# Kernel tuning notes

Hardware: AMD Instinct MI355X
Metric: run time of the kernel (lower is better)

The kernel has to match this reference:

```python
import jax, jax.numpy as jnp
import numpy as np

D_H = 1024

def _binary_operator(e_i, e_j):
    a_i, kv_i = e_i
    a_j, kv_j = e_j
    return (a_j * a_i, a_j * kv_i + kv_j)

def setup_inputs() -> dict:
    key = jax.random.key(0)
    k1, k2 = jax.random.split(key)
    B, S, D = 4, 4096, 1024
    x = jax.random.normal(k1, (B, S, D), dtype=jnp.float32)
    # nn.Dense default lecun_normal-ish scale; plain scaled normal is fine for a reference
    W = jax.random.normal(k2, (D, 3 * D_H), dtype=jnp.float32) * (1.0 / np.sqrt(D))
    b = jnp.zeros((3 * D_H,), dtype=jnp.float32)
    return {"x": x, "W": W, "b": b}

def reference(x, W, b):
    # projection: (B,S,D) @ (D, 3*d_h)
    proj = jnp.einsum('bsd,dh->bsh', x, W) + b
    inp = jnp.tanh(proj[:, :, :D_H])                 # (B,S,d_h)
    gates = jax.nn.sigmoid(proj[:, :, D_H:])         # (B,S,2*d_h)
    input_gate, output_gate = jnp.split(gates, 2, axis=-1)
    forget_gate = 1.0 - input_gate                   # tied gates
    _, hidden = jax.lax.associative_scan(
        _binary_operator, (forget_gate, inp * input_gate), axis=1)
    return jnp.tanh(hidden) * output_gate            # (B,S,d_h)
```

## Files before the change

### kernel.cpp

```cpp
#include <hip/hip_runtime.h>
#include <hip/hip_bf16.h>
#include <cmath>

typedef _Float16 half8 __attribute__((ext_vector_type(8)));
typedef _Float16 half4 __attribute__((ext_vector_type(4)));
typedef float f32x4 __attribute__((ext_vector_type(4)));

#define M_DIM 16384
#define K_DIM 1024
#define N_DIM 3072
#define S_LEN 4096
#define NCHUNK 64
#define CLEN 64

__device__ __forceinline__ float sigmoid_f(float x) {
    return 1.0f / (1.0f + __expf(-x));
}

__global__ void k_cast_x(const float* __restrict__ x, _Float16* __restrict__ xb) {
    int i = blockIdx.x * blockDim.x + threadIdx.x;
    float4 v = reinterpret_cast<const float4*>(x)[i];
    half4 h;
    h.x = (_Float16)v.x; h.y = (_Float16)v.y;
    h.z = (_Float16)v.z; h.w = (_Float16)v.w;
    reinterpret_cast<half4*>(xb)[i] = h;
}

__global__ void k_cast_w(const float* __restrict__ W, _Float16* __restrict__ Wt) {
    int t = blockIdx.x * blockDim.x + threadIdx.x;
    int n = t >> 10;
    int k = t & 1023;
    Wt[t] = (_Float16)W[(size_t)k * N_DIM + n];
}

__global__ __launch_bounds__(256, 2) void k_gemm(
    const _Float16* __restrict__ A,
    const _Float16* __restrict__ Bt,
    const float* __restrict__ bias,
    _Float16* __restrict__ G)
{
    __shared__ _Float16 As[128 * 64];
    __shared__ _Float16 Bs[128 * 64];

    const int lane = threadIdx.x & 63;
    const int w    = threadIdx.x >> 6;
    const int wr   = w >> 1;
    const int wc   = w & 1;

    const int bid   = blockIdx.x;
    const int tileM = (bid / 24) * 128;
    const int tileN = (bid % 24) * 128;

    f32x4 acc[4][4] = {};

    const int rsub = lane >> 3;
    const int ksub = (lane & 7) * 8;

    for (int kt = 0; kt < 16; ++kt) {
        __syncthreads();
        #pragma unroll
        for (int c = 0; c < 4; ++c) {
            const int row = w * 32 + c * 8 + rsub;
            const _Float16* gA = A  + (size_t)(tileM + row) * K_DIM + kt * 64 + ksub;
            const _Float16* gB = Bt + (size_t)(tileN + row) * K_DIM + kt * 64 + ksub;
            __builtin_amdgcn_global_load_lds(
                (const __attribute__((address_space(1))) void*)gA,
                (__attribute__((address_space(3))) void*)(As + (w * 32 + c * 8) * 64),
                16, 0, 0);
            __builtin_amdgcn_global_load_lds(
                (const __attribute__((address_space(1))) void*)gB,
                (__attribute__((address_space(3))) void*)(Bs + (w * 32 + c * 8) * 64),
                16, 0, 0);
        }
        __syncthreads();

        #pragma unroll
        for (int ks = 0; ks < 2; ++ks) {
            half8 af[4], bf[4];
            #pragma unroll
            for (int i = 0; i < 4; ++i)
                af[i] = *reinterpret_cast<const half8*>(
                    &As[(wr * 64 + i * 16 + (lane & 15)) * 64 + ks * 32 + (lane >> 4) * 8]);
            #pragma unroll
            for (int j = 0; j < 4; ++j)
                bf[j] = *reinterpret_cast<const half8*>(
                    &Bs[(wc * 64 + j * 16 + (lane & 15)) * 64 + ks * 32 + (lane >> 4) * 8]);
            #pragma unroll
            for (int i = 0; i < 4; ++i)
                #pragma unroll
                for (int j = 0; j < 4; ++j)
                    acc[i][j] = __builtin_amdgcn_mfma_f32_16x16x32_f16(
                        af[i], bf[j], acc[i][j], 0, 0, 0);
        }
    }

    #pragma unroll
    for (int j = 0; j < 4; ++j) {
        const int n = tileN + wc * 64 + j * 16 + (lane & 15);
        const float bn = bias[n];
        const bool is_tanh = (n < 1024);
        #pragma unroll
        for (int i = 0; i < 4; ++i) {
            const int mbase = tileM + wr * 64 + i * 16 + (lane >> 4) * 4;
            #pragma unroll
            for (int r = 0; r < 4; ++r) {
                float v = acc[i][j][r] + bn;
                float o = is_tanh ? tanhf(v) : sigmoid_f(v);
                G[(size_t)(mbase + r) * N_DIM + n] = (_Float16)o;
            }
        }
    }
}

__global__ void k_scan1(const _Float16* __restrict__ G,
                        float* __restrict__ sumA, float* __restrict__ sumH) {
    const int gid   = blockIdx.x;
    const int dblk  = gid & 3;
    const int chunk = (gid >> 2) & 63;
    const int b     = gid >> 8;
    const int d     = dblk * 256 + threadIdx.x;

    const _Float16* base = G + (size_t)(b * S_LEN + chunk * CLEN) * N_DIM;
    float A = 1.0f, H = 0.0f;
    #pragma unroll 4
    for (int s = 0; s < CLEN; ++s) {
        float g0 = (float)base[(size_t)s * N_DIM + d];
        float g1 = (float)base[(size_t)s * N_DIM + 1024 + d];
        float a  = 1.0f - g1;
        float kv = g0 * g1;
        H = fmaf(a, H, kv);
        A *= a;
    }
    const int cidx = (b * NCHUNK + chunk) * 1024 + d;
    sumA[cidx] = A;
    sumH[cidx] = H;
}

__global__ void k_scan2(const float* __restrict__ sumA, const float* __restrict__ sumH,
                        float* __restrict__ pref) {
    const int c = blockIdx.x * blockDim.x + threadIdx.x;
    const int b = c >> 10;
    const int d = c & 1023;
    float h = 0.0f;
    #pragma unroll 8
    for (int chunk = 0; chunk < NCHUNK; ++chunk) {
        const int idx = (b * NCHUNK + chunk) * 1024 + d;
        pref[idx] = h;
        h = fmaf(sumA[idx], h, sumH[idx]);
    }
}

__global__ void k_scan3(const _Float16* __restrict__ G,
                        const float* __restrict__ pref,
                        float* __restrict__ out) {
    const int gid   = blockIdx.x;
    const int dblk  = gid & 3;
    const int chunk = (gid >> 2) & 63;
    const int b     = gid >> 8;
    const int d     = dblk * 256 + threadIdx.x;

    const _Float16* base = G + (size_t)(b * S_LEN + chunk * CLEN) * N_DIM;
    float h = pref[(b * NCHUNK + chunk) * 1024 + d];
    #pragma unroll 4
    for (int s = 0; s < CLEN; ++s) {
        float g0 = (float)base[(size_t)s * N_DIM + d];
        float g1 = (float)base[(size_t)s * N_DIM + 1024 + d];
        float g2 = (float)base[(size_t)s * N_DIM + 2048 + d];
        float a  = 1.0f - g1;
        float kv = g0 * g1;
        h = fmaf(a, h, kv);
        out[(size_t)(b * S_LEN + chunk * CLEN + s) * 1024 + d] = tanhf(h) * g2;
    }
}

extern "C" void kernel_launch(void* const* d_in, const int* in_sizes, int n_in,
                              void* d_out, int out_size, void* d_ws, size_t ws_size,
                              hipStream_t stream) {
    const float* x = (const float*)d_in[0];
    const float* W = (const float*)d_in[1];
    const float* b = (const float*)d_in[2];
    float* out = (float*)d_out;

    char* ws = (char*)d_ws;
    _Float16* xb = (_Float16*)ws;
    _Float16* Wt = (_Float16*)(ws + 33554432);
    _Float16* G  = (_Float16*)(ws + 33554432 + 6291456);
    float* sumA  = (float*)(ws + 140509184);
    float* sumH  = sumA + 4096 * NCHUNK;
    float* pref  = sumH + 4096 * NCHUNK;

    k_cast_x<<<16384, 256, 0, stream>>>(x, xb);
    k_cast_w<<<12288, 256, 0, stream>>>(W, Wt);
    k_gemm <<<3072, 256, 0, stream>>>(xb, Wt, b, G);
    k_scan1<<<1024, 256, 0, stream>>>(G, sumA, sumH);
    k_scan2<<<16,   256, 0, stream>>>(sumA, sumH, pref);
    k_scan3<<<1024, 256, 0, stream>>>(G, pref, out);
    (void)in_sizes; (void)n_in; (void)out_size; (void)ws_size;
}
```

Measured before the change: 234.3 us.

## Triple-buffer GEMM with XOR-swizzled LDS, larger tiles, and tiled W transpose

The GEMM moves to 256x128 tiles with 512 threads, a three-slot LDS ring filled by global_load_lds, prefetch two k-steps ahead, and one barrier per step. LDS columns are XOR-swizzled to avoid bank conflicts, block IDs are remapped for L2 locality, and MFMA runs under raised wave priority. The W cast/transpose now goes through a shared-memory tile so both global reads and writes are coalesced. The cost is 144KB of dynamic LDS per block, which limits occupancy, plus more complex vmcnt bookkeeping.

Result: no change. 230.6 us (-1.6%).

```diff
diff --git a/kernel.cpp b/kernel.cpp
--- a/kernel.cpp
+++ b/kernel.cpp
@@ -12,6 +12,13 @@
 #define S_LEN 4096
 #define NCHUNK 64
 #define CLEN 64
+
+#define BM 256
+#define BN 128
+#define BK 64
+#define NT 16
+#define A_E 16384
+#define SLOT_E 24576
 
 __device__ __forceinline__ float sigmoid_f(float x) {
     return 1.0f / (1.0f + __expf(-x));
@@ -27,86 +34,127 @@
 }
 
 __global__ void k_cast_w(const float* __restrict__ W, _Float16* __restrict__ Wt) {
-    int t = blockIdx.x * blockDim.x + threadIdx.x;
-    int n = t >> 10;
-    int k = t & 1023;
-    Wt[t] = (_Float16)W[(size_t)k * N_DIM + n];
-}
-
-__global__ __launch_bounds__(256, 2) void k_gemm(
+    __shared__ float t[64][65];
+    const int k0 = (blockIdx.x / 48) * 64;
+    const int n0 = (blockIdx.x % 48) * 64;
+    const int c  = threadIdx.x & 63;
+    const int r0 = threadIdx.x >> 6;
+    #pragma unroll
+    for (int i = 0; i < 16; ++i) {
+        int r = r0 + i * 4;
+        t[r][c] = W[(size_t)(k0 + r) * N_DIM + n0 + c];
+    }
+    __syncthreads();
+    #pragma unroll
+    for (int i = 0; i < 16; ++i) {
+        int r = r0 + i * 4;
+        Wt[(size_t)(n0 + r) * K_DIM + k0 + c] = (_Float16)t[c][r];
+    }
+}
+
+__global__ __launch_bounds__(512, 2) void k_gemm(
     const _Float16* __restrict__ A,
     const _Float16* __restrict__ Bt,
     const float* __restrict__ bias,
     _Float16* __restrict__ G)
 {
-    __shared__ _Float16 As[128 * 64];
-    __shared__ _Float16 Bs[128 * 64];
-
-    const int lane = threadIdx.x & 63;
-    const int w    = threadIdx.x >> 6;
-    const int wr   = w >> 1;
-    const int wc   = w & 1;
+    extern __shared__ _Float16 lds[];
+
+    const int tid  = threadIdx.x;
+    const int lane = tid & 63;
+    const int wid  = tid >> 6;
+    const int wr   = wid >> 1;
+    const int wc   = wid & 1;
 
     const int bid   = blockIdx.x;
-    const int tileM = (bid / 24) * 128;
-    const int tileN = (bid % 24) * 128;
+    const int wg    = (bid & 7) * 192 + (bid >> 3);
+    const int tileM = (wg / 24) * BM;
+    const int tileN = (wg % 24) * BN;
+
+    const int l3   = lane >> 3;
+    const int c8   = lane & 7;
+    const int scol = ((c8 ^ l3) << 3);
+    const _Float16* gA = A  + (size_t)(tileM + wid * 8 + l3) * K_DIM + scol;
+    const _Float16* gB = Bt + (size_t)(tileN + wid * 8 + l3) * K_DIM + scol;
+
+    const int l15 = lane & 15;
+    const int hi  = lane >> 4;
+    const int swz = (l15 & 7) << 3;
+    const int o0  = (hi * 8)      ^ swz;
+    const int o1  = (32 + hi * 8) ^ swz;
 
     f32x4 acc[4][4] = {};
 
-    const int rsub = lane >> 3;
-    const int ksub = (lane & 7) * 8;
-
-    for (int kt = 0; kt < 16; ++kt) {
-        __syncthreads();
+#define GL(SRC, DST) __builtin_amdgcn_global_load_lds( \
+        (const __attribute__((address_space(1))) void*)(SRC), \
+        (__attribute__((address_space(3))) void*)(DST), 16, 0, 0)
+
+#define STAGE(kt, slot) do { \
+        _Float16* as_ = lds + (slot) * SLOT_E + wid * 512; \
+        _Float16* bs_ = lds + (slot) * SLOT_E + A_E + wid * 512; \
+        const _Float16* ga_ = gA + (size_t)(kt) * BK; \
+        const _Float16* gb_ = gB + (size_t)(kt) * BK; \
+        GL(ga_,                        as_);          \
+        GL(ga_ +  64 * K_DIM,          as_ + 4096);   \
+        GL(ga_ + 128 * K_DIM,          as_ + 8192);   \
+        GL(ga_ + 192 * K_DIM,          as_ + 12288);  \
+        GL(gb_,                        bs_);          \
+        GL(gb_ +  64 * K_DIM,          bs_ + 4096);   \
+    } while (0)
+
+    STAGE(0, 0);
+    STAGE(1, 1);
+    asm volatile("s_waitcnt vmcnt(6)" ::: "memory");
+    __builtin_amdgcn_s_barrier();
+
+    int sC = 0, sS = 2;
+    #pragma unroll 1
+    for (int t = 0; t < NT; ++t) {
+        if (t + 2 < NT) STAGE(t + 2, sS);
+
+        const _Float16* as = lds + sC * SLOT_E + (wr * 64 + l15) * 64;
+        const _Float16* bs = lds + sC * SLOT_E + A_E + (wc * 64 + l15) * 64;
+        half8 a0[4], a1[4], b0[4], b1[4];
         #pragma unroll
-        for (int c = 0; c < 4; ++c) {
-            const int row = w * 32 + c * 8 + rsub;
-            const _Float16* gA = A  + (size_t)(tileM + row) * K_DIM + kt * 64 + ksub;
-            const _Float16* gB = Bt + (size_t)(tileN + row) * K_DIM + kt * 64 + ksub;
-            __builtin_amdgcn_global_load_lds(
-                (const __attribute__((address_space(1))) void*)gA,
-                (__attribute__((address_space(3))) void*)(As + (w * 32 + c * 8) * 64),
-                16, 0, 0);
-            __builtin_amdgcn_global_load_lds(
-                (const __attribute__((address_space(1))) void*)gB,
-                (__attribute__((address_space(3))) void*)(Bs + (w * 32 + c * 8) * 64),
-                16, 0, 0);
+        for (int i = 0; i < 4; ++i) {
+            a0[i] = *(const half8*)(as + i * 1024 + o0);
+            a1[i] = *(const half8*)(as + i * 1024 + o1);
+            b0[i] = *(const half8*)(bs + i * 1024 + o0);
+            b1[i] = *(const half8*)(bs + i * 1024 + o1);
         }
-        __syncthreads();
-
+
+        __builtin_amdgcn_s_setprio(1);
         #pragma unroll
-        for (int ks = 0; ks < 2; ++ks) {
-            half8 af[4], bf[4];
+        for (int i = 0; i < 4; ++i)
             #pragma unroll
-            for (int i = 0; i < 4; ++i)
-                af[i] = *reinterpret_cast<const half8*>(
-                    &As[(wr * 64 + i * 16 + (lane & 15)) * 64 + ks * 32 + (lane >> 4) * 8]);
-            #pragma unroll
-            for (int j = 0; j < 4; ++j)
-                bf[j] = *reinterpret_cast<const half8*>(
-                    &Bs[(wc * 64 + j * 16 + (lane & 15)) * 64 + ks * 32 + (lane >> 4) * 8]);
-            #pragma unroll
-            for (int i = 0; i < 4; ++i)
-                #pragma unroll
-                for (int j = 0; j < 4; ++j)
-                    acc[i][j] = __builtin_amdgcn_mfma_f32_16x16x32_f16(
-                        af[i], bf[j], acc[i][j], 0, 0, 0);
-        }
-    }
+            for (int j = 0; j < 4; ++j) {
+                acc[i][j] = __builtin_amdgcn_mfma_f32_16x16x32_f16(a0[i], b0[j], acc[i][j], 0, 0, 0);
+                acc[i][j] = __builtin_amdgcn_mfma_f32_16x16x32_f16(a1[i], b1[j], acc[i][j], 0, 0, 0);
+            }
+        __builtin_amdgcn_s_setprio(0);
+
+        if (t < NT - 2)       asm volatile("s_waitcnt vmcnt(6)" ::: "memory");
+        else if (t == NT - 2) asm volatile("s_waitcnt vmcnt(0)" ::: "memory");
+        if (t < NT - 1) __builtin_amdgcn_s_barrier();
+
+        if (++sC == 3) sC = 0;
+        if (++sS == 3) sS = 0;
+    }
+#undef STAGE
+#undef GL
 
     #pragma unroll
     for (int j = 0; j < 4; ++j) {
-        const int n = tileN + wc * 64 + j * 16 + (lane & 15);
+        const int n = tileN + wc * 64 + j * 16 + l15;
         const float bn = bias[n];
         const bool is_tanh = (n < 1024);
         #pragma unroll
         for (int i = 0; i < 4; ++i) {
-            const int mbase = tileM + wr * 64 + i * 16 + (lane >> 4) * 4;
+            const int mb = tileM + wr * 64 + i * 16 + hi * 4;
             #pragma unroll
             for (int r = 0; r < 4; ++r) {
                 float v = acc[i][j][r] + bn;
-                float o = is_tanh ? tanhf(v) : sigmoid_f(v);
-                G[(size_t)(mbase + r) * N_DIM + n] = (_Float16)o;
+                G[(size_t)(mb + r) * N_DIM + n] = (_Float16)(is_tanh ? tanhf(v) : sigmoid_f(v));
             }
         }
     }
@@ -190,8 +238,8 @@
     float* pref  = sumH + 4096 * NCHUNK;
 
     k_cast_x<<<16384, 256, 0, stream>>>(x, xb);
-    k_cast_w<<<12288, 256, 0, stream>>>(W, Wt);
-    k_gemm <<<3072, 256, 0, stream>>>(xb, Wt, b, G);
+    k_cast_w<<<768,   256, 0, stream>>>(W, Wt);
+    k_gemm <<<1536, 512, 3 * SLOT_E * sizeof(_Float16), stream>>>(xb, Wt, b, G);
     k_scan1<<<1024, 256, 0, stream>>>(G, sumA, sumH);
     k_scan2<<<16,   256, 0, stream>>>(sumA, sumH, pref);
     k_scan3<<<1024, 256, 0, stream>>>(G, pref, out);
```
